# Performance work log

Hardware: AMD Instinct MI355X
Metric: run time of the kernel (lower is better)

## Reference

```python
import jax, jax.numpy as jnp
import numpy as np

B, T, C, H = 4, 4096, 1024, 128

def setup_inputs() -> dict:
    key = jax.random.key(0)
    k1, k2, k3, k4 = jax.random.split(key, 4)
    x = jax.random.normal(k1, (B, T, C), dtype=jnp.float32)
    # nn.Linear(embed, head, bias=False): y = x @ W, store W as [C, H]
    s = 1.0 / np.sqrt(C)
    Wk = jax.random.normal(k2, (C, H), dtype=jnp.float32) * s
    Wq = jax.random.normal(k3, (C, H), dtype=jnp.float32) * s
    Wv = jax.random.normal(k4, (C, H), dtype=jnp.float32) * s
    return {"x": x, "Wk": Wk, "Wq": Wq, "Wv": Wv}

def reference(x, Wk, Wq, Wv):
    Bx, Tx, Cx = x.shape
    scale = Wk.shape[1] ** -0.5
    k = x @ Wk  # [B,T,H]
    q = x @ Wq
    v = x @ Wv
    att = jnp.einsum('bth,bsh->bts', q, k) * scale  # [B,T,T]
    causal = jnp.triu(jnp.ones((Tx, Tx), dtype=bool), k=1)
    att = jnp.where(causal, -jnp.inf, att)
    att = jax.nn.softmax(att, axis=-1)
    # dropout is identity in eval mode
    out = jnp.einsum('bts,bsh->bth', att, v)  # [B,T,H]
    return out
```

## Files before the change

### kernel.cpp

```cpp
#include <hip/hip_runtime.h>
#include <stdint.h>
#include <math.h>

#define B_ 4
#define T_ 4096
#define C_ 1024
#define H_ 128

typedef __attribute__((ext_vector_type(8))) short s16x8;
typedef __attribute__((ext_vector_type(4))) float f32x4;

__device__ __forceinline__ unsigned short f2bf(float f) {
    union { float f; unsigned u; } v; v.f = f;
    unsigned r = v.u + 0x7fffu + ((v.u >> 16) & 1u);
    return (unsigned short)(r >> 16);
}

__device__ __forceinline__ s16x8 as_frag(uint4 u) {
    union { uint4 u; s16x8 s; } v; v.u = u; return v.s;
}

__host__ __device__ constexpr int chunks_total(int CH) {
    int a = 64 / CH, b = 64 % CH;
    return CH * a * (a + 1) / 2 + b * (a + 1);
}

#define QSC (0.0883883476f * 1.4426950408f)

__global__ __launch_bounds__(256) void k_wt(const float* __restrict__ Wk,
                                            const float* __restrict__ Wq,
                                            const float* __restrict__ Wv,
                                            unsigned short* __restrict__ Wt) {
    __shared__ float tile[64][65];
    int w = blockIdx.z;
    const float* W = (w == 0) ? Wk : (w == 1) ? Wq : Wv;
    int c0 = blockIdx.x * 64, h0 = blockIdx.y * 64;
    int tid = threadIdx.x;
#pragma unroll
    for (int k = 0; k < 16; k++) {
        int idx = tid + k * 256;
        int r = idx >> 6, c = idx & 63;
        tile[r][c] = W[(size_t)(c0 + r) * H_ + h0 + c];
    }
    __syncthreads();
#pragma unroll
    for (int k = 0; k < 16; k++) {
        int idx = tid + k * 256;
        int hh = idx >> 6, cc = idx & 63;
        Wt[(size_t)(w * H_ + h0 + hh) * C_ + c0 + cc] = f2bf(tile[cc][hh]);
    }
}

__global__ __launch_bounds__(256, 3) void k_qkv(const float* __restrict__ x,
                                                const unsigned short* __restrict__ Wt,
                                                unsigned short* __restrict__ Qb,
                                                unsigned short* __restrict__ Kb,
                                                unsigned short* __restrict__ Vt) {
    __shared__ unsigned short a_lds[2][64 * 72];
    int tid = threadIdx.x;
    int wv = tid >> 6, lane = tid & 63, quad = lane >> 4, lo = lane & 15;
    int r0 = blockIdx.x * 64;
    int cb = blockIdx.y;
    int nt0 = wv * 3;

    f32x4 acc[3][4];
#pragma unroll
    for (int i = 0; i < 3; i++)
#pragma unroll
        for (int j = 0; j < 4; j++) acc[i][j] = (f32x4){0.f, 0.f, 0.f, 0.f};

    const int row_s = tid >> 2;
    const int seg_s = (tid & 3) * 16;
    size_t xbase = (size_t)(r0 + row_s) * C_ + seg_s;

    const unsigned short* wp[3];
#pragma unroll
    for (int nt = 0; nt < 3; nt++)
        wp[nt] = Wt + (size_t)(cb * 192 + (nt0 + nt) * 16 + lo) * C_ + quad * 8;

    auto pack_store = [&](unsigned short* buf, const float4 (&f)[4]) {
        uint4 u0, u1;
        u0.x = (unsigned)f2bf(f[0].x) | ((unsigned)f2bf(f[0].y) << 16);
        u0.y = (unsigned)f2bf(f[0].z) | ((unsigned)f2bf(f[0].w) << 16);
        u0.z = (unsigned)f2bf(f[1].x) | ((unsigned)f2bf(f[1].y) << 16);
        u0.w = (unsigned)f2bf(f[1].z) | ((unsigned)f2bf(f[1].w) << 16);
        u1.x = (unsigned)f2bf(f[2].x) | ((unsigned)f2bf(f[2].y) << 16);
        u1.y = (unsigned)f2bf(f[2].z) | ((unsigned)f2bf(f[2].w) << 16);
        u1.z = (unsigned)f2bf(f[3].x) | ((unsigned)f2bf(f[3].y) << 16);
        u1.w = (unsigned)f2bf(f[3].z) | ((unsigned)f2bf(f[3].w) << 16);
        *(uint4*)&buf[row_s * 72 + seg_s] = u0;
        *(uint4*)&buf[row_s * 72 + seg_s + 8] = u1;
    };
    auto load_x = [&](float4 (&f)[4], int kc) {
        const float* xp = x + xbase + kc * 64;
#pragma unroll
        for (int j = 0; j < 4; j++) f[j] = *(const float4*)(xp + j * 4);
    };
    auto compute = [&](const unsigned short* buf, int kc) {
        s16x8 b[3][2];
#pragma unroll
        for (int nt = 0; nt < 3; nt++)
#pragma unroll
            for (int kh = 0; kh < 2; kh++)
                b[nt][kh] = *(const s16x8*)(wp[nt] + kc * 64 + kh * 32);
        s16x8 af[4][2];
#pragma unroll
        for (int mt = 0; mt < 4; mt++)
#pragma unroll
            for (int kh = 0; kh < 2; kh++)
                af[mt][kh] = *(const s16x8*)&buf[(mt * 16 + lo) * 72 + kh * 32 + quad * 8];
#pragma unroll
        for (int nt = 0; nt < 3; nt++)
#pragma unroll
            for (int kh = 0; kh < 2; kh++)
#pragma unroll
                for (int mt = 0; mt < 4; mt++)
                    acc[nt][mt] = __builtin_amdgcn_mfma_f32_16x16x32_bf16(
                        af[mt][kh], b[nt][kh], acc[nt][mt], 0, 0, 0);
    };

    float4 x0[4], x1[4];
    load_x(x0, 0);
    load_x(x1, 1);
    pack_store(a_lds[0], x0);
    __syncthreads();

    for (int kc2 = 0; kc2 < 8; kc2++) {
        int kc = kc2 * 2;
        if (kc + 2 < 16) load_x(x0, kc + 2);
        compute(a_lds[0], kc);
        pack_store(a_lds[1], x1);
        __syncthreads();
        if (kc + 3 < 16) load_x(x1, kc + 3);
        compute(a_lds[1], kc + 1);
        if (kc + 2 < 16) pack_store(a_lds[0], x0);
        __syncthreads();
    }

#pragma unroll
    for (int nt = 0; nt < 3; nt++) {
        int col = cb * 192 + (nt0 + nt) * 16 + lo;
        int w = col >> 7, h = col & 127;
#pragma unroll
        for (int mt = 0; mt < 4; mt++) {
            int mrow = r0 + mt * 16 + quad * 4;
            if (w == 2) {
                int b = mrow >> 12, t0 = mrow & 4095;
                int tp = (t0 & ~31) + (((t0 & 15) >> 2) << 3) + (((t0 >> 4) & 1) << 2);
                uint2 pk;
                pk.x = (unsigned)f2bf(acc[nt][mt][0]) | ((unsigned)f2bf(acc[nt][mt][1]) << 16);
                pk.y = (unsigned)f2bf(acc[nt][mt][2]) | ((unsigned)f2bf(acc[nt][mt][3]) << 16);
                *(uint2*)(Vt + (size_t)(b * H_ + h) * T_ + tp) = pk;
            } else if (w == 1) {
                unsigned short* dst = Qb + (size_t)mrow * H_ + h;
#pragma unroll
                for (int r = 0; r < 4; r++)
                    dst[(size_t)r * H_] = f2bf(acc[nt][mt][r] * QSC);
            } else {
                unsigned short* dst = Kb + (size_t)mrow * H_ + h;
#pragma unroll
                for (int r = 0; r < 4; r++)
                    dst[(size_t)r * H_] = f2bf(acc[nt][mt][r]);
            }
        }
    }
}

#define LOAD_KV(kv0)                                                            \
    do {                                                                        \
        const uint4* kg = (const uint4*)(Kb + (size_t)(batch * T_ + (kv0) + srow_k) * H_); \
        pk0 = kg[sseg_k + 0]; pk1 = kg[sseg_k + 1];                             \
        pk2 = kg[sseg_k + 2]; pk3 = kg[sseg_k + 3];                             \
        const uint4* vg = (const uint4*)(Vt + (size_t)(batch * H_ + srow_v) * T_ + (kv0)); \
        pv0 = vg[sseg_v + 0]; pv1 = vg[sseg_v + 1];                             \
        pv2 = vg[sseg_v + 2]; pv3 = vg[sseg_v + 3];                             \
    } while (0)

template <int CH>
__global__ __launch_bounds__(256, 4) void k_attn(const unsigned short* __restrict__ Qb,
                                                 const unsigned short* __restrict__ Kb,
                                                 const unsigned short* __restrict__ Vt,
                                                 float* __restrict__ Opart,
                                                 float* __restrict__ Mpart,
                                                 float* __restrict__ Lpart,
                                                 float* __restrict__ out) {
    __shared__ uint4 kbuf[64 * 16];
    __shared__ uint4 vbuf[128 * 8];

    int tid = threadIdx.x;
    int wv = tid >> 6, lane = tid & 63, quad = lane >> 4, lo = lane & 15;

    int id = blockIdx.x;
    int qt, batch, tbeg, tend, slot = 0;
    if constexpr (CH > 0) {
        slot = id >> 2; batch = id & 3;
        int s = slot, q = 63;
        for (;;) { int nc = (q + CH) / CH; if (s < nc) break; s -= nc; --q; }
        qt = q;
        tbeg = s * CH;
        tend = min(tbeg + CH, qt + 1);
    } else {
        qt = 63 - (id >> 2); batch = id & 3;
        tbeg = 0; tend = qt + 1;
    }
    int m0 = qt * 64 + wv * 16;
    int query = m0 + lo;

    s16x8 qf[4];
    size_t qrow = (size_t)(batch * T_ + m0 + lo) * H_;
#pragma unroll
    for (int ks = 0; ks < 4; ks++)
        qf[ks] = *(const s16x8*)(Qb + qrow + ks * 32 + quad * 8);

    f32x4 acc_o[8];
#pragma unroll
    for (int o = 0; o < 8; o++) acc_o[o] = (f32x4){0.f, 0.f, 0.f, 0.f};
    float m_i = -INFINITY, l_i = 0.f;

    const int srow_k = tid >> 2, sseg_k = (tid & 3) * 4;
    const int srow_v = tid >> 1, sseg_v = (tid & 1) * 4;

    uint4 pk0, pk1, pk2, pk3, pv0, pv1, pv2, pv3;
    LOAD_KV(tbeg * 64);

    for (int t = tbeg; t < tend; ++t) {
        int kv0 = t * 64;
        kbuf[srow_k * 16 + ((sseg_k + 0) ^ (srow_k & 15))] = pk0;
        kbuf[srow_k * 16 + ((sseg_k + 1) ^ (srow_k & 15))] = pk1;
        kbuf[srow_k * 16 + ((sseg_k + 2) ^ (srow_k & 15))] = pk2;
        kbuf[srow_k * 16 + ((sseg_k + 3) ^ (srow_k & 15))] = pk3;
        vbuf[srow_v * 8 + ((sseg_v + 0) ^ (srow_v & 7))] = pv0;
        vbuf[srow_v * 8 + ((sseg_v + 1) ^ (srow_v & 7))] = pv1;
        vbuf[srow_v * 8 + ((sseg_v + 2) ^ (srow_v & 7))] = pv2;
        vbuf[srow_v * 8 + ((sseg_v + 3) ^ (srow_v & 7))] = pv3;
        __syncthreads();
        if (t + 1 < tend) LOAD_KV((t + 1) * 64);

        f32x4 s_acc[4];
#pragma unroll
        for (int nt = 0; nt < 4; nt++) s_acc[nt] = (f32x4){0.f, 0.f, 0.f, 0.f};
        __builtin_amdgcn_s_setprio(1);
#pragma unroll
        for (int ks = 0; ks < 4; ks++) {
#pragma unroll
            for (int nt = 0; nt < 4; nt++) {
                s16x8 kf = as_frag(kbuf[(nt * 16 + lo) * 16 + ((ks * 4 + quad) ^ lo)]);
                s_acc[nt] = __builtin_amdgcn_mfma_f32_16x16x32_bf16(kf, qf[ks], s_acc[nt], 0, 0, 0);
            }
        }
        __builtin_amdgcn_s_setprio(0);

        float p[4][4];
#pragma unroll
        for (int nt = 0; nt < 4; nt++)
#pragma unroll
            for (int r = 0; r < 4; r++) p[nt][r] = s_acc[nt][r];
        if (t == qt) {
#pragma unroll
            for (int nt = 0; nt < 4; nt++)
#pragma unroll
                for (int r = 0; r < 4; r++)
                    if (kv0 + nt * 16 + quad * 4 + r > query) p[nt][r] = -INFINITY;
        }

        float mx = p[0][0];
#pragma unroll
        for (int nt = 0; nt < 4; nt++)
#pragma unroll
            for (int r = 0; r < 4; r++) mx = fmaxf(mx, p[nt][r]);
        if (__any(mx > m_i + 8.0f)) {
            float rm = fmaxf(mx, __shfl_xor(mx, 16));
            rm = fmaxf(rm, __shfl_xor(rm, 32));
            float mnew = fmaxf(m_i, rm);
            float alpha = exp2f(m_i - mnew);
            l_i *= alpha;
            m_i = mnew;
#pragma unroll
            for (int o = 0; o < 8; o++)
#pragma unroll
                for (int r = 0; r < 4; r++) acc_o[o][r] *= alpha;
        }
        float rs = 0.f;
#pragma unroll
        for (int nt = 0; nt < 4; nt++)
#pragma unroll
            for (int r = 0; r < 4; r++) {
                float pv = exp2f(p[nt][r] - m_i);
                p[nt][r] = pv;
                rs += pv;
            }
        l_i += rs;

        s16x8 pf[2];
#pragma unroll
        for (int kt = 0; kt < 2; kt++) {
            uint4 u;
            u.x = (__float_as_uint(p[2 * kt][0]) >> 16) | ((__float_as_uint(p[2 * kt][1]) >> 16) << 16);
            u.y = (__float_as_uint(p[2 * kt][2]) >> 16) | ((__float_as_uint(p[2 * kt][3]) >> 16) << 16);
            u.z = (__float_as_uint(p[2 * kt + 1][0]) >> 16) | ((__float_as_uint(p[2 * kt + 1][1]) >> 16) << 16);
            u.w = (__float_as_uint(p[2 * kt + 1][2]) >> 16) | ((__float_as_uint(p[2 * kt + 1][3]) >> 16) << 16);
            pf[kt] = as_frag(u);
        }

        __builtin_amdgcn_s_setprio(1);
#pragma unroll
        for (int kt = 0; kt < 2; kt++)
#pragma unroll
            for (int o = 0; o < 8; o++) {
                int vrow = o * 16 + lo;
                s16x8 vf = as_frag(vbuf[vrow * 8 + ((kt * 4 + quad) ^ (vrow & 7))]);
                acc_o[o] = __builtin_amdgcn_mfma_f32_16x16x32_bf16(vf, pf[kt], acc_o[o], 0, 0, 0);
            }
        __builtin_amdgcn_s_setprio(0);
        __syncthreads();
    }

    l_i += __shfl_xor(l_i, 16);
    l_i += __shfl_xor(l_i, 32);

    if constexpr (CH > 0) {
        constexpr int NCH = chunks_total(CH);
        size_t pr = (size_t)(batch * NCH + slot) * 64 + wv * 16 + lo;
        float* Op = Opart + pr * 128;
#pragma unroll
        for (int o = 0; o < 8; o++) {
            float4 v = {acc_o[o][0], acc_o[o][1], acc_o[o][2], acc_o[o][3]};
            *(float4*)(Op + o * 16 + quad * 4) = v;
        }
        if (quad == 0) { Mpart[pr] = m_i; Lpart[pr] = l_i; }
    } else {
        float inv = 1.0f / l_i;
        int rowg = batch * T_ + m0 + lo;
#pragma unroll
        for (int o = 0; o < 8; o++) {
            float4 v = {acc_o[o][0] * inv, acc_o[o][1] * inv,
                        acc_o[o][2] * inv, acc_o[o][3] * inv};
            *(float4*)(out + (size_t)rowg * H_ + o * 16 + quad * 4) = v;
        }
    }
}

template <int CH>
__global__ __launch_bounds__(256) void k_comb(const float* __restrict__ Opart,
                                              const float* __restrict__ Mpart,
                                              const float* __restrict__ Lpart,
                                              float* __restrict__ out) {
    constexpr int NCH = chunks_total(CH);
    int tid = threadIdx.x;
    int row = blockIdx.x * 8 + (tid >> 5);
    int h4 = (tid & 31) * 4;
    int batch = row >> 12, t = row & 4095, qt = t >> 6;
    int n = qt + 1;
    int nc = (qt + CH) / CH;
    int a = n / CH, b = n % CH;
    int S = CH * a * (a + 1) / 2 + b * (a + 1);
    int base = NCH - S;
    float M = -INFINITY, den = 0.f;
    float4 o = {0.f, 0.f, 0.f, 0.f};
    for (int s = 0; s < nc; ++s) {
        size_t pr = (size_t)(batch * NCH + base + s) * 64 + (t & 63);
        float ms = Mpart[pr], ls = Lpart[pr];
        float4 v = *(const float4*)(Opart + pr * 128 + h4);
        float Mn = fmaxf(M, ms);
        float wa = exp2f(M - Mn), wb = exp2f(ms - Mn);
        den = den * wa + ls * wb;
        o.x = o.x * wa + v.x * wb;
        o.y = o.y * wa + v.y * wb;
        o.z = o.z * wa + v.z * wb;
        o.w = o.w * wa + v.w * wb;
        M = Mn;
    }
    float inv = 1.0f / den;
    float4 r = {o.x * inv, o.y * inv, o.z * inv, o.w * inv};
    *(float4*)(out + (size_t)row * H_ + h4) = r;
}

extern "C" void kernel_launch(void* const* d_in, const int* in_sizes, int n_in,
                              void* d_out, int out_size, void* d_ws, size_t ws_size,
                              hipStream_t stream) {
    const float* x  = (const float*)d_in[0];
    const float* Wk = (const float*)d_in[1];
    const float* Wq = (const float*)d_in[2];
    const float* Wv = (const float*)d_in[3];
    char* ws = (char*)d_ws;
    unsigned short* Wt = (unsigned short*)ws;
    unsigned short* Qb = (unsigned short*)(ws + (1u << 20));
    unsigned short* Kb = (unsigned short*)(ws + (5u << 20));
    unsigned short* Vt = (unsigned short*)(ws + (9u << 20));
    float* out = (float*)d_out;

    const size_t base = (size_t)13 << 20;
    constexpr int NCH10 = chunks_total(10);
    constexpr int NCH21 = chunks_total(21);
    auto need_for = [&](int nch) {
        return base + (size_t)4 * nch * 64 * (128 * 4) + 2 * (size_t)4 * nch * 64 * 4;
    };

    k_wt  <<<dim3(16, 2, 3), 256, 0, stream>>>(Wk, Wq, Wv, Wt);
    k_qkv <<<dim3(256, 2), 256, 0, stream>>>(x, Wt, Qb, Kb, Vt);

    if (ws_size >= need_for(NCH10)) {
        float* Op = (float*)(ws + base);
        float* Mp = Op + (size_t)4 * NCH10 * 64 * 128;
        float* Lp = Mp + (size_t)4 * NCH10 * 64;
        k_attn<10><<<4 * NCH10, 256, 0, stream>>>(Qb, Kb, Vt, Op, Mp, Lp, out);
        k_comb<10><<<2048, 256, 0, stream>>>(Op, Mp, Lp, out);
    } else if (ws_size >= need_for(NCH21)) {
        float* Op = (float*)(ws + base);
        float* Mp = Op + (size_t)4 * NCH21 * 64 * 128;
        float* Lp = Mp + (size_t)4 * NCH21 * 64;
        k_attn<21><<<4 * NCH21, 256, 0, stream>>>(Qb, Kb, Vt, Op, Mp, Lp, out);
        k_comb<21><<<2048, 256, 0, stream>>>(Op, Mp, Lp, out);
    } else {
        k_attn<0><<<256, 256, 0, stream>>>(Qb, Kb, Vt, nullptr, nullptr, nullptr, out);
    }
}
```

Baseline: 174.6 us.

## Split QKV projection K dimension across two wave groups with LDS reduction

The QKV projection kernel now launches 512 threads per block. Two groups of four waves each handle one half of the C=1024 reduction dimension, so each group runs 8 k-chunks instead of 16. The two partial accumulators are summed through LDS in two rounds before only the first group writes output. This aims to raise parallelism and latency hiding in the projection stage, which has only 512 blocks. The cost is doubled LDS for A tiles, an extra reduction phase with barriers, and higher register pressure under the tighter launch bounds.

```diff
diff --git a/kernel.cpp b/kernel.cpp
--- a/kernel.cpp
+++ b/kernel.cpp
@@ -51,17 +51,18 @@
     }
 }
 
-__global__ __launch_bounds__(256, 3) void k_qkv(const float* __restrict__ x,
+__global__ __launch_bounds__(512, 4) void k_qkv(const float* __restrict__ x,
                                                 const unsigned short* __restrict__ Wt,
                                                 unsigned short* __restrict__ Qb,
                                                 unsigned short* __restrict__ Kb,
                                                 unsigned short* __restrict__ Vt) {
-    __shared__ unsigned short a_lds[2][64 * 72];
+    __shared__ unsigned short a_lds[2][2][64 * 72];
     int tid = threadIdx.x;
     int wv = tid >> 6, lane = tid & 63, quad = lane >> 4, lo = lane & 15;
+    int half = wv >> 2, wvl = wv & 3;
     int r0 = blockIdx.x * 64;
     int cb = blockIdx.y;
-    int nt0 = wv * 3;
+    int nt0 = wvl * 3;
 
     f32x4 acc[3][4];
 #pragma unroll
@@ -69,14 +70,15 @@
 #pragma unroll
         for (int j = 0; j < 4; j++) acc[i][j] = (f32x4){0.f, 0.f, 0.f, 0.f};
 
-    const int row_s = tid >> 2;
-    const int seg_s = (tid & 3) * 16;
-    size_t xbase = (size_t)(r0 + row_s) * C_ + seg_s;
+    const int tidh = tid & 255;
+    const int row_s = tidh >> 2;
+    const int seg_s = (tidh & 3) * 16;
+    size_t xbase = (size_t)(r0 + row_s) * C_ + half * 512 + seg_s;
 
     const unsigned short* wp[3];
 #pragma unroll
     for (int nt = 0; nt < 3; nt++)
-        wp[nt] = Wt + (size_t)(cb * 192 + (nt0 + nt) * 16 + lo) * C_ + quad * 8;
+        wp[nt] = Wt + (size_t)(cb * 192 + (nt0 + nt) * 16 + lo) * C_ + half * 512 + quad * 8;
 
     auto pack_store = [&](unsigned short* buf, const float4 (&f)[4]) {
         uint4 u0, u1;
@@ -119,23 +121,49 @@
                         af[mt][kh], b[nt][kh], acc[nt][mt], 0, 0, 0);
     };
 
-    float4 x0[4], x1[4];
-    load_x(x0, 0);
-    load_x(x1, 1);
-    pack_store(a_lds[0], x0);
+    float4 xr[4];
+    load_x(xr, 0);
+    pack_store(&a_lds[0][half][0], xr);
     __syncthreads();
 
-    for (int kc2 = 0; kc2 < 8; kc2++) {
-        int kc = kc2 * 2;
-        if (kc + 2 < 16) load_x(x0, kc + 2);
-        compute(a_lds[0], kc);
-        pack_store(a_lds[1], x1);
+#pragma unroll 1
+    for (int kc = 0; kc < 8; kc++) {
+        float4 xn[4];
+        if (kc < 7) load_x(xn, kc + 1);
+        compute(&a_lds[kc & 1][half][0], kc);
+        if (kc < 7) pack_store(&a_lds[(kc & 1) ^ 1][half][0], xn);
         __syncthreads();
-        if (kc + 3 < 16) load_x(x1, kc + 3);
-        compute(a_lds[1], kc + 1);
-        if (kc + 2 < 16) pack_store(a_lds[0], x0);
+    }
+
+    float* red = (float*)&a_lds[0][0][0];
+    const int slot = (wvl * 64 + lane) * 6;
+#pragma unroll
+    for (int rd = 0; rd < 2; rd++) {
+        if (half == 1) {
+#pragma unroll
+            for (int i = 0; i < 6; i++) {
+                const int fi = rd * 6 + i;
+                float4 v = {acc[fi >> 2][fi & 3][0], acc[fi >> 2][fi & 3][1],
+                            acc[fi >> 2][fi & 3][2], acc[fi >> 2][fi & 3][3]};
+                *(float4*)&red[(size_t)(slot + i) * 4] = v;
+            }
+        }
         __syncthreads();
-    }
+        if (half == 0) {
+#pragma unroll
+            for (int i = 0; i < 6; i++) {
+                const int fi = rd * 6 + i;
+                float4 v = *(const float4*)&red[(size_t)(slot + i) * 4];
+                acc[fi >> 2][fi & 3][0] += v.x;
+                acc[fi >> 2][fi & 3][1] += v.y;
+                acc[fi >> 2][fi & 3][2] += v.z;
+                acc[fi >> 2][fi & 3][3] += v.w;
+            }
+        }
+        __syncthreads();
+    }
+
+    if (half != 0) return;
 
 #pragma unroll
     for (int nt = 0; nt < 3; nt++) {
@@ -397,7 +425,7 @@
     };
 
     k_wt  <<<dim3(16, 2, 3), 256, 0, stream>>>(Wk, Wq, Wv, Wt);
-    k_qkv <<<dim3(256, 2), 256, 0, stream>>>(x, Wt, Qb, Kb, Vt);
+    k_qkv <<<dim3(256, 2), 512, 0, stream>>>(x, Wt, Qb, Kb, Vt);
 
     if (ws_size >= need_for(NCH10)) {
         float* Op = (float*)(ws + base);
```

Measured after the change: 173.6 us. Within noise of the previous version (-0.6%).
